# Performance work log

Measured on AMD Instinct MI355X. Metric: run time of the kernel, lower is better.

## Reference

```python
import jax, jax.numpy as jnp
import numpy as np
import math

HEADS = 8
DIM_HEAD = 64


def setup_inputs() -> dict:
    key = jax.random.key(0)
    k1, k2, k3 = jax.random.split(key, 3)
    b, n, dim = 4, 2048, 512
    inner = HEADS * DIM_HEAD  # 512
    x = jax.random.normal(k1, (b, n, dim), dtype=jnp.float32)
    W_qkv = jax.random.normal(k2, (dim, 4 * inner), dtype=jnp.float32) * (dim ** -0.5)
    W_out = jax.random.normal(k3, (2 * inner, dim), dtype=jnp.float32) * ((2 * inner) ** -0.5)
    b_out = jnp.zeros((dim,), dtype=jnp.float32)
    return {"x": x, "W_qkv": W_qkv, "W_out": W_out, "b_out": b_out}


def reference(x, W_qkv, W_out, b_out):
    b, n, d = x.shape
    h, dh = HEADS, DIM_HEAD
    scale = dh ** -0.5
    qkvt = x @ W_qkv  # [b, n, 4*h*dh]
    q, k, v, t = jnp.split(qkvt, 4, axis=-1)
    # 'b n (h d) -> b h n d'
    def to_heads(z):
        return z.reshape(b, n, h, dh).transpose(0, 2, 1, 3)
    q, k, v, t = map(to_heads, (q, k, v, t))

    # Branch 1: standard softmax attention
    dots = jnp.einsum('bhid,bhjd->bhij', q, k) * scale
    attn1 = jax.nn.softmax(dots, axis=-1)
    out1 = jnp.einsum('bhij,bhjd->bhid', attn1, v)

    # Branch 2: fixed positional-decay attention (shared across b, h; no repeat needed)
    pos = jnp.arange(1, n + 1, dtype=x.dtype)  # linspace(1, n, n)
    tg = jnp.abs(pos[None, :] - pos[:, None])  # |j - i|, [n, n]
    attn2 = jnp.exp(-tg / jnp.asarray(math.e, dtype=x.dtype))
    # NOTE: original divides by sum(-1) WITHOUT keepdim -> broadcasts over columns:
    # attn2[i, j] / sum_k attn2[j, k]
    attn2 = attn2 / attn2.sum(-1)
    out2 = jnp.einsum('ij,bhjd->bhid', attn2, t)

    out = jnp.concatenate([out1, out2], axis=-1)  # [b, h, n, 2*dh]
    out = out.transpose(0, 2, 1, 3).reshape(b, n, 2 * h * dh)  # 'b h n d -> b n (h d)'
    return out @ W_out + b_out
```

## Files before the change

### kernel.cpp

```cpp
#include <hip/hip_runtime.h>
#include <hip/hip_bf16.h>

#define B_ 4
#define N_ 2048
#define D_ 512
#define H_ 8
#define DH_ 64

typedef float float4_ __attribute__((ext_vector_type(4)));
typedef int int2_ __attribute__((ext_vector_type(2)));
typedef int int4_ __attribute__((ext_vector_type(4)));
typedef unsigned short ushort4_ __attribute__((ext_vector_type(4)));
typedef unsigned short ushort8_ __attribute__((ext_vector_type(8)));
typedef __bf16 bf16x8 __attribute__((ext_vector_type(8)));
typedef _Float16 half2_ __attribute__((ext_vector_type(2)));
typedef _Float16 half4_ __attribute__((ext_vector_type(4)));
typedef _Float16 half8_ __attribute__((ext_vector_type(8)));

#if __has_builtin(__builtin_amdgcn_exp2f)
#define EXP2(x) __builtin_amdgcn_exp2f(x)
#else
#define EXP2(x) exp2f(x)
#endif

__device__ __forceinline__ float b2f(unsigned short u) {
  union { unsigned int u; float f; } v; v.u = ((unsigned int)u) << 16; return v.f;
}
__device__ __forceinline__ unsigned short f2b(float f) {
  union { float f; unsigned int u; } v; v.f = f;
  unsigned int r = v.u + 0x7fffu + ((v.u >> 16) & 1u);
  return (unsigned short)(r >> 16);
}
__device__ __forceinline__ half4_ pk4(float a, float b, float c, float d) {
  half2_ lo = __builtin_bit_cast(half2_, __builtin_amdgcn_cvt_pkrtz(a, b));
  half2_ hi = __builtin_bit_cast(half2_, __builtin_amdgcn_cvt_pkrtz(c, d));
  return __builtin_bit_cast(half4_,
      (int2_){__builtin_bit_cast(int, lo), __builtin_bit_cast(int, hi)});
}

#define GLD16(gp, lp)                                                        \
  __builtin_amdgcn_global_load_lds(                                          \
      (const __attribute__((address_space(1))) unsigned int*)(gp),           \
      (__attribute__((address_space(3))) unsigned int*)(lp), 16, 0, 0)

__global__ __launch_bounds__(256) void detect_fp32(
    const unsigned short* __restrict__ x, int* __restrict__ flag) {
  __shared__ int cnt;
  if (threadIdx.x == 0) cnt = 0;
  __syncthreads();
  int local = 0;
  for (int i = threadIdx.x; i < 4096; i += 256) {
    ushort4_ v = ((const ushort4_*)x)[i];
#pragma unroll
    for (int e = 0; e < 4; ++e)
      if (((v[e] >> 7) & 0xFFu) >= 134u) local++;
  }
  atomicAdd(&cnt, local);
  __syncthreads();
  if (threadIdx.x == 0) *flag = (cnt > 100) ? 1 : 0;
}

__global__ __launch_bounds__(256) void convert_all(
    const void* __restrict__ s0, const void* __restrict__ s1,
    const void* __restrict__ s2, const void* __restrict__ s3,
    unsigned short* __restrict__ d0, unsigned short* __restrict__ d1,
    unsigned short* __restrict__ d2, unsigned short* __restrict__ d3,
    const int* __restrict__ flag) {
  int i4 = blockIdx.x * 256 + threadIdx.x;
  const void* src; unsigned short* dst; int off;
  if (i4 < 1048576)      { src = s0; dst = d0; off = i4; }
  else if (i4 < 1310720) { src = s1; dst = d1; off = i4 - 1048576; }
  else if (i4 < 1441792) { src = s2; dst = d2; off = i4 - 1310720; }
  else if (i4 < 1441920) { src = s3; dst = d3; off = i4 - 1441792; }
  else return;
  ushort4_ o;
  if (*flag) {
    float4_ v = *(const float4_*)((const float*)src + (long)off * 4);
    o[0] = f2b(v[0]); o[1] = f2b(v[1]); o[2] = f2b(v[2]); o[3] = f2b(v[3]);
  } else {
    o = *(const ushort4_*)((const unsigned short*)src + (long)off * 4);
  }
  *(ushort4_*)(dst + (long)off * 4) = o;
}

__device__ __forceinline__ void transpose_body(
    const unsigned short* __restrict__ src, unsigned short* __restrict__ dst,
    int R, int C, int bx, int by) {
  __shared__ unsigned short tile[32][33];
  const int c0 = bx * 32, r0 = by * 32;
  const int tx = threadIdx.x & 31, ty = threadIdx.x >> 5;
#pragma unroll
  for (int k = 0; k < 4; ++k) {
    int r = ty + k * 8;
    tile[r][tx] = src[(long)(r0 + r) * C + c0 + tx];
  }
  __syncthreads();
#pragma unroll
  for (int k = 0; k < 4; ++k) {
    int c = ty + k * 8;
    dst[(long)(c0 + c) * R + r0 + tx] = tile[tx][c];
  }
}

__global__ __launch_bounds__(256) void prep_misc(
    const unsigned short* __restrict__ Wqb, unsigned short* __restrict__ WqT,
    const unsigned short* __restrict__ Wob, unsigned short* __restrict__ WoT,
    unsigned short* __restrict__ Wband) {
  const int bid = blockIdx.x;
  if (bid < 1024) {
    transpose_body(Wqb, WqT, 512, 2048, bid % 64, bid / 64);
  } else if (bid < 1536) {
    const int b2 = bid - 1024;
    transpose_body(Wob, WoT, 1024, 512, b2 % 16, b2 / 16);
  } else {
    constexpr float INV_E = 0.36787944117144233f;
    constexpr float R1 = 0.69220062755534635f;
    constexpr float INV_1MR = 3.2488706f;
    const int i = bid - 1536;
    const int krel = threadIdx.x;
    const int j = (i >> 6) * 64 - 96 + krel;
    float c = 0.f;
    if (j >= 0 && j < N_) {
      float wgt = __expf(-fabsf((float)(i - j)) * INV_E);
      float rj = __expf(-(float)j * INV_E);
      float rnj = __expf(-(float)(N_ - 1 - j) * INV_E);
      float S = 1.f + R1 * (2.f - rj - rnj) * INV_1MR;
      c = wgt / S;
    }
    _Float16 hv = (_Float16)c;
    Wband[i * 256 + krel] = __builtin_bit_cast(unsigned short, hv);
  }
}

__global__ __launch_bounds__(256) void gemm128(
    const unsigned short* __restrict__ A, const unsigned short* __restrict__ Bt,
    void* __restrict__ C, const unsigned short* __restrict__ bias,
    int M, int N, int K, const int* __restrict__ ofp32) {
  __shared__ unsigned short As[128 * 32];
  __shared__ unsigned short Bs[128 * 32];
  const int tid = threadIdx.x;
  const int w = tid >> 6, lane = tid & 63, l16 = lane & 15, quad = lane >> 4;
  const int wm = (w & 1) * 64, wn = (w >> 1) * 64;
  const long tm = (long)blockIdx.x * 128, tn = (long)blockIdx.y * 128;
  const int srow = w * 32 + (lane >> 2);
  const int scol = (lane & 3) * 8;
  float4_ acc[4][4] = {};
  for (int k0 = 0; k0 < K; k0 += 32) {
#pragma unroll
    for (int q = 0; q < 2; ++q) {
      GLD16(&A[(tm + srow + q * 16) * K + k0 + scol], &As[(w * 32 + q * 16) * 32]);
      GLD16(&Bt[(tn + srow + q * 16) * K + k0 + scol], &Bs[(w * 32 + q * 16) * 32]);
    }
    __syncthreads();
    bf16x8 af[4], bf[4];
#pragma unroll
    for (int mb = 0; mb < 4; ++mb)
      af[mb] = __builtin_bit_cast(bf16x8,
          *(const int4_*)&As[(wm + mb * 16 + l16) * 32 + quad * 8]);
#pragma unroll
    for (int nb = 0; nb < 4; ++nb)
      bf[nb] = __builtin_bit_cast(bf16x8,
          *(const int4_*)&Bs[(wn + nb * 16 + l16) * 32 + quad * 8]);
#pragma unroll
    for (int mb = 0; mb < 4; ++mb)
#pragma unroll
      for (int nb = 0; nb < 4; ++nb)
        acc[mb][nb] = __builtin_amdgcn_mfma_f32_16x16x32_bf16(
            af[mb], bf[nb], acc[mb][nb], 0, 0, 0);
    __syncthreads();
  }
  const bool ofp = ofp32 && (*ofp32 != 0);
#pragma unroll
  for (int nb = 0; nb < 4; ++nb) {
    long col = tn + wn + nb * 16 + l16;
    float bv = bias ? b2f(bias[col]) : 0.f;
#pragma unroll
    for (int mb = 0; mb < 4; ++mb)
#pragma unroll
      for (int r = 0; r < 4; ++r) {
        long row = tm + wm + mb * 16 + quad * 4 + r;
        float val = acc[mb][nb][r] + bv;
        if (ofp) ((float*)C)[row * N + col] = val;
        else ((unsigned short*)C)[row * N + col] = f2b(val);
      }
  }
}

__global__ __launch_bounds__(256) void gemm_n64(
    const unsigned short* __restrict__ A, const unsigned short* __restrict__ Bt,
    void* __restrict__ C, const unsigned short* __restrict__ bias,
    int M, int N, int K, const int* __restrict__ ofp32) {
  __shared__ unsigned short As[128 * 32];
  __shared__ unsigned short Bs[64 * 32];
  const int tid = threadIdx.x;
  const int w = tid >> 6, lane = tid & 63, l16 = lane & 15, quad = lane >> 4;
  const int wm = (w & 1) * 64, wn = (w >> 1) * 32;
  const long tm = (long)blockIdx.x * 128, tn = (long)blockIdx.y * 64;
  const int srowA = w * 32 + (lane >> 2);
  const int srowB = w * 16 + (lane >> 2);
  const int scol = (lane & 3) * 8;
  float4_ acc[4][2] = {};
  for (int k0 = 0; k0 < K; k0 += 32) {
#pragma unroll
    for (int q = 0; q < 2; ++q)
      GLD16(&A[(tm + srowA + q * 16) * K + k0 + scol], &As[(w * 32 + q * 16) * 32]);
    GLD16(&Bt[(tn + srowB) * K + k0 + scol], &Bs[(w * 16) * 32]);
    __syncthreads();
    bf16x8 af[4], bf[2];
#pragma unroll
    for (int mb = 0; mb < 4; ++mb)
      af[mb] = __builtin_bit_cast(bf16x8,
          *(const int4_*)&As[(wm + mb * 16 + l16) * 32 + quad * 8]);
#pragma unroll
    for (int nb = 0; nb < 2; ++nb)
      bf[nb] = __builtin_bit_cast(bf16x8,
          *(const int4_*)&Bs[(wn + nb * 16 + l16) * 32 + quad * 8]);
#pragma unroll
    for (int mb = 0; mb < 4; ++mb)
#pragma unroll
      for (int nb = 0; nb < 2; ++nb)
        acc[mb][nb] = __builtin_amdgcn_mfma_f32_16x16x32_bf16(
            af[mb], bf[nb], acc[mb][nb], 0, 0, 0);
    __syncthreads();
  }
  const bool ofp = ofp32 && (*ofp32 != 0);
#pragma unroll
  for (int nb = 0; nb < 2; ++nb) {
    long col = tn + wn + nb * 16 + l16;
    float bv = bias ? b2f(bias[col]) : 0.f;
#pragma unroll
    for (int mb = 0; mb < 4; ++mb)
#pragma unroll
      for (int r = 0; r < 4; ++r) {
        long row = tm + wm + mb * 16 + quad * 4 + r;
        float val = acc[mb][nb][r] + bv;
        if (ofp) ((float*)C)[row * N + col] = val;
        else ((unsigned short*)C)[row * N + col] = f2b(val);
      }
  }
}

#define TTW 2240
__global__ __launch_bounds__(256) void build_vtt(
    const unsigned short* __restrict__ qkvt, unsigned short* __restrict__ Vt,
    unsigned short* __restrict__ Tt) {
  const int z = blockIdx.z;
  if (z == 4) {
    int bid = blockIdx.y * 64 + blockIdx.x;
    int idx4 = (bid * 256 + threadIdx.x) * 4;
    if (idx4 >= 2048 * 192) return;
    int row = idx4 / 192, rem = idx4 % 192;
    int pos = (rem < 96) ? rem : (rem - 96) + 96 + 2048;
    *(ushort4_*)&Tt[(long)row * TTW + pos] = (ushort4_){0, 0, 0, 0};
    return;
  }
  __shared__ unsigned short tile[32][33];
  const int bh = blockIdx.y, b = bh >> 3, h = bh & 7;
  const int j0 = blockIdx.x * 32;
  const bool isv = (z < 2);
  const int d0 = (isv ? z : z - 2) * 32;
  const int srccol = isv ? 1024 : 1536;
  const int tx = threadIdx.x & 31, ty = threadIdx.x >> 5;
#pragma unroll
  for (int k = 0; k < 4; ++k) {
    int j = ty + k * 8;
    tile[j][tx] = qkvt[(long)(b * N_ + j0 + j) * 2048 + srccol + h * 64 + d0 + tx];
  }
  __syncthreads();
#pragma unroll
  for (int k = 0; k < 4; ++k) {
    int dd = ty + k * 8;
    _Float16 hv = (_Float16)b2f(tile[tx][dd]);
    unsigned short us = __builtin_bit_cast(unsigned short, hv);
    if (isv)
      Vt[((long)bh * 64 + d0 + dd) * 2048 + j0 + tx] = us;
    else
      Tt[((long)bh * 64 + d0 + dd) * TTW + 96 + j0 + tx] = us;
  }
}

__global__ __launch_bounds__(256) void branch2_mfma(
    const unsigned short* __restrict__ Wband, const unsigned short* __restrict__ Tt,
    unsigned short* __restrict__ catb) {
  const int qtile = blockIdx.x;
  const int bh = blockIdx.y, b = bh >> 3, h = bh & 7;
  const int tid = threadIdx.x;
  const int w = tid >> 6, lane = tid & 63, l16 = lane & 15, quad = lane >> 4;
  const int i_row = qtile * 64 + w * 16 + l16;
  const unsigned short* ap = Wband + i_row * 256;
  float4_ acc[4] = {};
#pragma unroll
  for (int kh = 0; kh < 8; ++kh) {
    half8_ af = __builtin_bit_cast(half8_, *(const int4_*)&ap[kh * 32 + quad * 8]);
#pragma unroll
    for (int nb = 0; nb < 4; ++nb) {
      half8_ bf = __builtin_bit_cast(half8_,
          *(const int4_*)&Tt[((long)bh * 64 + nb * 16 + l16) * TTW +
                             qtile * 64 + kh * 32 + quad * 8]);
      acc[nb] = __builtin_amdgcn_mfma_f32_16x16x32_f16(af, bf, acc[nb], 0, 0, 0);
    }
  }
#pragma unroll
  for (int nb = 0; nb < 4; ++nb)
#pragma unroll
    for (int r = 0; r < 4; ++r) {
      int row = qtile * 64 + w * 16 + quad * 4 + r;
      catb[(long)(b * N_ + row) * 1024 + h * 128 + 64 + nb * 16 + l16] =
          f2b(acc[nb][r]);
    }
}

__global__ __launch_bounds__(256) void flash_kernel(
    const unsigned short* __restrict__ qkvt, const unsigned short* __restrict__ Vt,
    unsigned short* __restrict__ catb) {
  __shared__ unsigned short Ks[2][64 * 64];
  __shared__ unsigned short Vs[2][64 * 64];
  const int bh = blockIdx.y, b = bh >> 3, h = bh & 7;
  const int i0 = blockIdx.x * 64;
  const int tid = threadIdx.x;
  const int w = tid >> 6, lane = tid & 63, l16 = lane & 15, quad = lane >> 4;
  const int srow8 = lane >> 3, sch = lane & 7;
  const int chK = sch ^ srow8;
  bf16x8 qf[2];
  {
    constexpr float SCL = 0.125f * 1.44269504088896f;
    const long qrow = (long)(b * N_ + i0 + w * 16 + l16) * 2048 + h * 64;
#pragma unroll
    for (int kh = 0; kh < 2; ++kh) {
      ushort8_ raw = __builtin_bit_cast(ushort8_,
          *(const int4_*)&qkvt[qrow + kh * 32 + quad * 8]);
      ushort8_ sc;
#pragma unroll
      for (int e = 0; e < 8; ++e) sc[e] = f2b(b2f(raw[e]) * SCL);
      qf[kh] = __builtin_bit_cast(bf16x8, sc);
    }
  }
  const unsigned short* kp[2];
#pragma unroll
  for (int kh = 0; kh < 2; ++kh)
    kp[kh] = &Ks[0][l16 * 64 + (((kh * 4 + quad) ^ (l16 & 7)) * 8)];
  const unsigned short* vp[4];
#pragma unroll
  for (int c = 0; c < 4; ++c)
    vp[c] = &Vs[0][l16 * 64 + (((c * 2 + (quad >> 1)) ^ (l16 & 7)) * 8) +
                   (quad & 1) * 4];
  const unsigned short* kg[2];
  const unsigned short* vg[2];
#pragma unroll
  for (int g = 0; g < 2; ++g) {
    const int row = w * 16 + g * 8 + srow8;
    kg[g] = qkvt + (long)(b * N_ + row) * 2048 + 512 + h * 64 + chK * 8;
    vg[g] = Vt + ((long)bh * 64 + row) * 2048 + chK * 8;
  }
  float4_ O[4] = {};
  float4_ O5 = {};
  const half4_ ones = {(_Float16)1.f, (_Float16)1.f, (_Float16)1.f, (_Float16)1.f};

  auto stage = [&](int jt_, int buf_) __attribute__((always_inline)) {
    const int j0 = jt_ * 64;
#pragma unroll
    for (int g = 0; g < 2; ++g) {
      GLD16(kg[g] + (long)j0 * 2048,
            (char*)&Ks[0][0] + buf_ * 8192 + (w * 16 + g * 8) * 128);
      GLD16(vg[g] + j0,
            (char*)&Vs[0][0] + buf_ * 8192 + (w * 16 + g * 8) * 128);
    }
  };
  auto phase = [&](int jt_, int buf_) __attribute__((always_inline)) {
    if (jt_ + 1 < 32) stage(jt_ + 1, buf_ ^ 1);
    float4_ s[4] = {};
#pragma unroll
    for (int kh = 0; kh < 2; ++kh)
#pragma unroll
      for (int c = 0; c < 4; ++c) {
        bf16x8 kf = __builtin_bit_cast(bf16x8,
            *(const int4_*)(kp[kh] + buf_ * 4096 + c * 1024));
        s[c] = __builtin_amdgcn_mfma_f32_16x16x32_bf16(kf, qf[kh], s[c], 0, 0, 0);
      }
    half4_ pf[4];
#pragma unroll
    for (int c = 0; c < 4; ++c)
      pf[c] = pk4(EXP2(s[c][0]), EXP2(s[c][1]), EXP2(s[c][2]), EXP2(s[c][3]));
#pragma unroll
    for (int c = 0; c < 4; ++c) {
#pragma unroll
      for (int dblk = 0; dblk < 4; ++dblk) {
        half4_ vfv = *(const half4_*)(vp[c] + buf_ * 4096 + dblk * 1024);
        O[dblk] = __builtin_amdgcn_mfma_f32_16x16x16f16(
            pf[c], vfv, O[dblk], 0, 0, 0);
      }
      O5 = __builtin_amdgcn_mfma_f32_16x16x16f16(pf[c], ones, O5, 0, 0, 0);
    }
    __syncthreads();
  };

  stage(0, 0);
  __syncthreads();
  for (int jt = 0; jt < 32; jt += 2) {
    phase(jt, 0);
    phase(jt + 1, 1);
  }
  float linv[4];
#pragma unroll
  for (int r = 0; r < 4; ++r) linv[r] = 1.f / O5[r];
#pragma unroll
  for (int dblk = 0; dblk < 4; ++dblk)
#pragma unroll
    for (int r = 0; r < 4; ++r) {
      int row = i0 + w * 16 + quad * 4 + r;
      catb[(long)(b * N_ + row) * 1024 + h * 128 + dblk * 16 + l16] =
          f2b(O[dblk][r] * linv[r]);
    }
}

extern "C" void kernel_launch(void* const* d_in, const int* in_sizes, int n_in,
                              void* d_out, int out_size, void* d_ws, size_t ws_size,
                              hipStream_t stream) {
  char* ws = (char*)d_ws;
  unsigned short* qkvt = (unsigned short*)(ws);
  unsigned short* WqT  = (unsigned short*)(ws + (size_t)32 * 1024 * 1024);
  unsigned short* WoT  = (unsigned short*)(ws + (size_t)34 * 1024 * 1024);
  unsigned short* Vt   = (unsigned short*)(ws + (size_t)35 * 1024 * 1024);
  unsigned short* catb = (unsigned short*)(ws + (size_t)43 * 1024 * 1024);
  unsigned short* xb   = (unsigned short*)(ws + (size_t)59 * 1024 * 1024);
  unsigned short* Wqb  = (unsigned short*)(ws + (size_t)67 * 1024 * 1024);
  unsigned short* Wob  = (unsigned short*)(ws + (size_t)69 * 1024 * 1024);
  unsigned short* bob  = (unsigned short*)(ws + (size_t)70 * 1024 * 1024);
  int* flag            = (int*)(ws + (size_t)70 * 1024 * 1024 + 4096);
  unsigned short* Wband= (unsigned short*)(ws + (size_t)70 * 1024 * 1024 + 8192);
  unsigned short* Tt   = xb;

  detect_fp32<<<1, 256, 0, stream>>>((const unsigned short*)d_in[0], flag);
  convert_all<<<5633, 256, 0, stream>>>(d_in[0], d_in[1], d_in[2], d_in[3],
                                        xb, Wqb, Wob, bob, flag);
  prep_misc<<<3584, 256, 0, stream>>>(Wqb, WqT, Wob, WoT, Wband);
  gemm128<<<dim3(8192 / 128, 2048 / 128), 256, 0, stream>>>(
      xb, WqT, qkvt, (const unsigned short*)nullptr, 8192, 2048, 512,
      (const int*)nullptr);
  build_vtt<<<dim3(64, 32, 5), 256, 0, stream>>>(qkvt, Vt, Tt);
  flash_kernel<<<dim3(2048 / 64, 32), 256, 0, stream>>>(qkvt, Vt, catb);
  branch2_mfma<<<dim3(32, 32), 256, 0, stream>>>(Wband, Tt, catb);
  gemm_n64<<<dim3(8192 / 128, 512 / 64), 256, 0, stream>>>(
      catb, WoT, d_out, bob, 8192, 512, 1024, flag);
}
```

Before: 228.3 us.

## Fuse input conversion, detection and transposes into one prep kernel; fold branch2 into flash

```diff
diff --git a/kernel.cpp b/kernel.cpp
--- a/kernel.cpp
+++ b/kernel.cpp
@@ -43,56 +43,28 @@
       (const __attribute__((address_space(1))) unsigned int*)(gp),           \
       (__attribute__((address_space(3))) unsigned int*)(lp), 16, 0, 0)
 
-__global__ __launch_bounds__(256) void detect_fp32(
-    const unsigned short* __restrict__ x, int* __restrict__ flag) {
-  __shared__ int cnt;
-  if (threadIdx.x == 0) cnt = 0;
+__device__ __forceinline__ bool detect_fp32_local(
+    const unsigned short* __restrict__ xhdr, int* cnt_sh) {
+  if (threadIdx.x == 0) *cnt_sh = 0;
   __syncthreads();
-  int local = 0;
-  for (int i = threadIdx.x; i < 4096; i += 256) {
-    ushort4_ v = ((const ushort4_*)x)[i];
-#pragma unroll
-    for (int e = 0; e < 4; ++e)
-      if (((v[e] >> 7) & 0xFFu) >= 134u) local++;
-  }
-  atomicAdd(&cnt, local);
+  unsigned int e = (xhdr[threadIdx.x] >> 7) & 0xFFu;
+  if (e >= 134u) atomicAdd(cnt_sh, 1);
   __syncthreads();
-  if (threadIdx.x == 0) *flag = (cnt > 100) ? 1 : 0;
-}
-
-__global__ __launch_bounds__(256) void convert_all(
-    const void* __restrict__ s0, const void* __restrict__ s1,
-    const void* __restrict__ s2, const void* __restrict__ s3,
-    unsigned short* __restrict__ d0, unsigned short* __restrict__ d1,
-    unsigned short* __restrict__ d2, unsigned short* __restrict__ d3,
-    const int* __restrict__ flag) {
-  int i4 = blockIdx.x * 256 + threadIdx.x;
-  const void* src; unsigned short* dst; int off;
-  if (i4 < 1048576)      { src = s0; dst = d0; off = i4; }
-  else if (i4 < 1310720) { src = s1; dst = d1; off = i4 - 1048576; }
-  else if (i4 < 1441792) { src = s2; dst = d2; off = i4 - 1310720; }
-  else if (i4 < 1441920) { src = s3; dst = d3; off = i4 - 1441792; }
-  else return;
-  ushort4_ o;
-  if (*flag) {
-    float4_ v = *(const float4_*)((const float*)src + (long)off * 4);
-    o[0] = f2b(v[0]); o[1] = f2b(v[1]); o[2] = f2b(v[2]); o[3] = f2b(v[3]);
-  } else {
-    o = *(const ushort4_*)((const unsigned short*)src + (long)off * 4);
-  }
-  *(ushort4_*)(dst + (long)off * 4) = o;
-}
-
-__device__ __forceinline__ void transpose_body(
-    const unsigned short* __restrict__ src, unsigned short* __restrict__ dst,
-    int R, int C, int bx, int by) {
+  return *cnt_sh > 16;
+}
+
+__device__ __forceinline__ void transpose_conv(
+    const void* __restrict__ src, unsigned short* __restrict__ dst,
+    int R, int C, int bx, int by, bool ofp) {
   __shared__ unsigned short tile[32][33];
   const int c0 = bx * 32, r0 = by * 32;
   const int tx = threadIdx.x & 31, ty = threadIdx.x >> 5;
 #pragma unroll
   for (int k = 0; k < 4; ++k) {
     int r = ty + k * 8;
-    tile[r][tx] = src[(long)(r0 + r) * C + c0 + tx];
+    long idx = (long)(r0 + r) * C + c0 + tx;
+    tile[r][tx] = ofp ? f2b(((const float*)src)[idx])
+                      : ((const unsigned short*)src)[idx];
   }
   __syncthreads();
 #pragma unroll
@@ -102,21 +74,35 @@
   }
 }
 
-__global__ __launch_bounds__(256) void prep_misc(
-    const unsigned short* __restrict__ Wqb, unsigned short* __restrict__ WqT,
-    const unsigned short* __restrict__ Wob, unsigned short* __restrict__ WoT,
+__global__ __launch_bounds__(256) void prep_all(
+    const void* __restrict__ xraw, const void* __restrict__ Wqraw,
+    const void* __restrict__ Woraw, unsigned short* __restrict__ xb,
+    unsigned short* __restrict__ WqT, unsigned short* __restrict__ WoT,
     unsigned short* __restrict__ Wband) {
+  __shared__ int cnt_sh;
+  const bool ofp = detect_fp32_local((const unsigned short*)xraw, &cnt_sh);
   const int bid = blockIdx.x;
-  if (bid < 1024) {
-    transpose_body(Wqb, WqT, 512, 2048, bid % 64, bid / 64);
-  } else if (bid < 1536) {
-    const int b2 = bid - 1024;
-    transpose_body(Wob, WoT, 1024, 512, b2 % 16, b2 / 16);
+  if (bid < 4096) {
+    int i4 = bid * 256 + threadIdx.x;
+    ushort4_ o;
+    if (ofp) {
+      float4_ v = ((const float4_*)xraw)[i4];
+      o[0] = f2b(v[0]); o[1] = f2b(v[1]); o[2] = f2b(v[2]); o[3] = f2b(v[3]);
+    } else {
+      o = ((const ushort4_*)xraw)[i4];
+    }
+    *(ushort4_*)(xb + (long)i4 * 4) = o;
+  } else if (bid < 5120) {
+    const int b2 = bid - 4096;
+    transpose_conv(Wqraw, WqT, 512, 2048, b2 % 64, b2 / 64, ofp);
+  } else if (bid < 5632) {
+    const int b2 = bid - 5120;
+    transpose_conv(Woraw, WoT, 1024, 512, b2 % 16, b2 / 16, ofp);
   } else {
     constexpr float INV_E = 0.36787944117144233f;
     constexpr float R1 = 0.69220062755534635f;
     constexpr float INV_1MR = 3.2488706f;
-    const int i = bid - 1536;
+    const int i = bid - 5632;
     const int krel = threadIdx.x;
     const int j = (i >> 6) * 64 - 96 + krel;
     float c = 0.f;
@@ -134,8 +120,7 @@
 
 __global__ __launch_bounds__(256) void gemm128(
     const unsigned short* __restrict__ A, const unsigned short* __restrict__ Bt,
-    void* __restrict__ C, const unsigned short* __restrict__ bias,
-    int M, int N, int K, const int* __restrict__ ofp32) {
+    unsigned short* __restrict__ C, int M, int N, int K) {
   __shared__ unsigned short As[128 * 32];
   __shared__ unsigned short Bs[128 * 32];
   const int tid = threadIdx.x;
@@ -169,27 +154,25 @@
             af[mb], bf[nb], acc[mb][nb], 0, 0, 0);
     __syncthreads();
   }
-  const bool ofp = ofp32 && (*ofp32 != 0);
 #pragma unroll
   for (int nb = 0; nb < 4; ++nb) {
     long col = tn + wn + nb * 16 + l16;
-    float bv = bias ? b2f(bias[col]) : 0.f;
 #pragma unroll
     for (int mb = 0; mb < 4; ++mb)
 #pragma unroll
       for (int r = 0; r < 4; ++r) {
         long row = tm + wm + mb * 16 + quad * 4 + r;
-        float val = acc[mb][nb][r] + bv;
-        if (ofp) ((float*)C)[row * N + col] = val;
-        else ((unsigned short*)C)[row * N + col] = f2b(val);
+        C[row * N + col] = f2b(acc[mb][nb][r]);
       }
   }
 }
 
 __global__ __launch_bounds__(256) void gemm_n64(
     const unsigned short* __restrict__ A, const unsigned short* __restrict__ Bt,
-    void* __restrict__ C, const unsigned short* __restrict__ bias,
-    int M, int N, int K, const int* __restrict__ ofp32) {
+    void* __restrict__ C, const void* __restrict__ bias_raw,
+    int M, int N, int K, const unsigned short* __restrict__ xhdr) {
+  __shared__ int cnt_sh;
+  const bool ofp = detect_fp32_local(xhdr, &cnt_sh);
   __shared__ unsigned short As[128 * 32];
   __shared__ unsigned short Bs[64 * 32];
   const int tid = threadIdx.x;
@@ -223,11 +206,11 @@
             af[mb], bf[nb], acc[mb][nb], 0, 0, 0);
     __syncthreads();
   }
-  const bool ofp = ofp32 && (*ofp32 != 0);
 #pragma unroll
   for (int nb = 0; nb < 2; ++nb) {
     long col = tn + wn + nb * 16 + l16;
-    float bv = bias ? b2f(bias[col]) : 0.f;
+    float bv = ofp ? ((const float*)bias_raw)[col]
+                   : b2f(((const unsigned short*)bias_raw)[col]);
 #pragma unroll
     for (int mb = 0; mb < 4; ++mb)
 #pragma unroll
@@ -279,39 +262,9 @@
   }
 }
 
-__global__ __launch_bounds__(256) void branch2_mfma(
-    const unsigned short* __restrict__ Wband, const unsigned short* __restrict__ Tt,
-    unsigned short* __restrict__ catb) {
-  const int qtile = blockIdx.x;
-  const int bh = blockIdx.y, b = bh >> 3, h = bh & 7;
-  const int tid = threadIdx.x;
-  const int w = tid >> 6, lane = tid & 63, l16 = lane & 15, quad = lane >> 4;
-  const int i_row = qtile * 64 + w * 16 + l16;
-  const unsigned short* ap = Wband + i_row * 256;
-  float4_ acc[4] = {};
-#pragma unroll
-  for (int kh = 0; kh < 8; ++kh) {
-    half8_ af = __builtin_bit_cast(half8_, *(const int4_*)&ap[kh * 32 + quad * 8]);
-#pragma unroll
-    for (int nb = 0; nb < 4; ++nb) {
-      half8_ bf = __builtin_bit_cast(half8_,
-          *(const int4_*)&Tt[((long)bh * 64 + nb * 16 + l16) * TTW +
-                             qtile * 64 + kh * 32 + quad * 8]);
-      acc[nb] = __builtin_amdgcn_mfma_f32_16x16x32_f16(af, bf, acc[nb], 0, 0, 0);
-    }
-  }
-#pragma unroll
-  for (int nb = 0; nb < 4; ++nb)
-#pragma unroll
-    for (int r = 0; r < 4; ++r) {
-      int row = qtile * 64 + w * 16 + quad * 4 + r;
-      catb[(long)(b * N_ + row) * 1024 + h * 128 + 64 + nb * 16 + l16] =
-          f2b(acc[nb][r]);
-    }
-}
-
 __global__ __launch_bounds__(256) void flash_kernel(
     const unsigned short* __restrict__ qkvt, const unsigned short* __restrict__ Vt,
+    const unsigned short* __restrict__ Wband, const unsigned short* __restrict__ Tt,
     unsigned short* __restrict__ catb) {
   __shared__ unsigned short Ks[2][64 * 64];
   __shared__ unsigned short Vs[2][64 * 64];
@@ -411,6 +364,31 @@
       catb[(long)(b * N_ + row) * 1024 + h * 128 + dblk * 16 + l16] =
           f2b(O[dblk][r] * linv[r]);
     }
+  {
+    const int qtile = blockIdx.x;
+    const int i_row = qtile * 64 + w * 16 + l16;
+    const unsigned short* ap = Wband + i_row * 256;
+    float4_ acc2[4] = {};
+#pragma unroll
+    for (int kh = 0; kh < 8; ++kh) {
+      half8_ af = __builtin_bit_cast(half8_, *(const int4_*)&ap[kh * 32 + quad * 8]);
+#pragma unroll
+      for (int nb = 0; nb < 4; ++nb) {
+        half8_ bf = __builtin_bit_cast(half8_,
+            *(const int4_*)&Tt[((long)bh * 64 + nb * 16 + l16) * TTW +
+                               qtile * 64 + kh * 32 + quad * 8]);
+        acc2[nb] = __builtin_amdgcn_mfma_f32_16x16x32_f16(af, bf, acc2[nb], 0, 0, 0);
+      }
+    }
+#pragma unroll
+    for (int nb = 0; nb < 4; ++nb)
+#pragma unroll
+      for (int r = 0; r < 4; ++r) {
+        int row = qtile * 64 + w * 16 + quad * 4 + r;
+        catb[(long)(b * N_ + row) * 1024 + h * 128 + 64 + nb * 16 + l16] =
+            f2b(acc2[nb][r]);
+      }
+  }
 }
 
 extern "C" void kernel_launch(void* const* d_in, const int* in_sizes, int n_in,
@@ -423,23 +401,17 @@
   unsigned short* Vt   = (unsigned short*)(ws + (size_t)35 * 1024 * 1024);
   unsigned short* catb = (unsigned short*)(ws + (size_t)43 * 1024 * 1024);
   unsigned short* xb   = (unsigned short*)(ws + (size_t)59 * 1024 * 1024);
-  unsigned short* Wqb  = (unsigned short*)(ws + (size_t)67 * 1024 * 1024);
-  unsigned short* Wob  = (unsigned short*)(ws + (size_t)69 * 1024 * 1024);
-  unsigned short* bob  = (unsigned short*)(ws + (size_t)70 * 1024 * 1024);
-  int* flag            = (int*)(ws + (size_t)70 * 1024 * 1024 + 4096);
-  unsigned short* Wband= (unsigned short*)(ws + (size_t)70 * 1024 * 1024 + 8192);
+  unsigned short* Wband= (unsigned short*)(ws + (size_t)68 * 1024 * 1024);
   unsigned short* Tt   = xb;
 
-  detect_fp32<<<1, 256, 0, stream>>>((const unsigned short*)d_in[0], flag);
-  convert_all<<<5633, 256, 0, stream>>>(d_in[0], d_in[1], d_in[2], d_in[3],
-                                        xb, Wqb, Wob, bob, flag);
-  prep_misc<<<3584, 256, 0, stream>>>(Wqb, WqT, Wob, WoT, Wband);
+  prep_all<<<7680, 256, 0, stream>>>(d_in[0], d_in[1], d_in[2],
+                                     xb, WqT, WoT, Wband);
   gemm128<<<dim3(8192 / 128, 2048 / 128), 256, 0, stream>>>(
-      xb, WqT, qkvt, (const unsigned short*)nullptr, 8192, 2048, 512,
-      (const int*)nullptr);
+      xb, WqT, qkvt, 8192, 2048, 512);
   build_vtt<<<dim3(64, 32, 5), 256, 0, stream>>>(qkvt, Vt, Tt);
-  flash_kernel<<<dim3(2048 / 64, 32), 256, 0, stream>>>(qkvt, Vt, catb);
-  branch2_mfma<<<dim3(32, 32), 256, 0, stream>>>(Wband, Tt, catb);
+  flash_kernel<<<dim3(2048 / 64, 32), 256, 0, stream>>>(
+      qkvt, Vt, Wband, Tt, catb);
   gemm_n64<<<dim3(8192 / 128, 512 / 64), 256, 0, stream>>>(
-      catb, WoT, d_out, bob, 8192, 512, 1024, flag);
-}
+      catb, WoT, d_out, d_in[3], 8192, 512, 1024,
+      (const unsigned short*)d_in[0]);
+}
```

Result: faster. 220.5 us (-3.4%).
